# Kernel optimization log

Measured on AMD Instinct MI355X. Metric: run time of the kernel, lower is better.

## Reference

```python
import jax, jax.numpy as jnp
import numpy as np

# Static configuration (matches init_kwargs)
B, C, H, W = 8, 64, 256, 256
WS = 8            # window size
HEADS = 4
DH = 16           # dim per head, HEADS*DH == C
L = WS * WS       # tokens per window
EPS_LN = 1e-5

# --- Swin relative-position index (static, numpy) ---
_coords = np.stack(np.meshgrid(np.arange(WS), np.arange(WS), indexing='ij'))  # [2,ws,ws]
_flat = _coords.reshape(2, -1)                                                # [2,L]
_rel = (_flat[:, :, None] - _flat[:, None, :]).transpose(1, 2, 0).copy()      # [L,L,2]
_rel[..., 0] += WS - 1
_rel[..., 1] += WS - 1
_rel[..., 0] *= 2 * WS - 1
REL_IDX = _rel.sum(-1)  # [L,L] ints in [0, (2ws-1)^2)


def _biasfree_ln(x, w):
    # x: [B,C,H,W]; BiasFree_LayerNorm over channel dim (biased var, no mean subtraction in scale)
    var = jnp.var(x, axis=1, keepdims=True)
    return x * jax.lax.rsqrt(var + EPS_LN) * w[None, :, None, None]


def _win_partition(t):  # [B,H,W,C] -> [N, L, C]
    t = t.reshape(B, H // WS, WS, W // WS, WS, C).transpose(0, 1, 3, 2, 4, 5)
    return t.reshape(-1, L, C)


def _win_reverse(t):  # [N, L, C] -> [B,H,W,C]
    t = t.reshape(B, H // WS, W // WS, WS, WS, C).transpose(0, 1, 3, 2, 4, 5)
    return t.reshape(B, H, W, C)


def _l2norm(t):
    # torch F.normalize(dim=-1) semantics
    n = jnp.sqrt(jnp.sum(t * t, axis=-1, keepdims=True))
    return t / jnp.maximum(n, 1e-12)


def _forward(x, illu_fea, ln1_w, ln2_w, w_qkv, b_qkv, rpb_table, w_proj, b_proj,
             temperature, w_qkv_m, w_dw, w_out_m):
    # ---------- spatial (window) attention branch ----------
    xs = _biasfree_ln(x, ln1_w).transpose(0, 2, 3, 1)          # [B,H,W,C]
    xw = _win_partition(xs)                                     # [N,L,C]
    iw = _win_partition(illu_fea.transpose(0, 2, 3, 1))         # [N,L,C]
    iw = iw.reshape(-1, L, HEADS, DH).transpose(0, 2, 1, 3)     # [N,h,L,d]

    qkv = (xw @ w_qkv + b_qkv).reshape(-1, L, 3, HEADS, DH).transpose(2, 0, 3, 1, 4)
    q, k, v = qkv[0], qkv[1], qkv[2]                            # [N,h,L,d]
    scale = DH ** (-0.5)
    attn = jnp.einsum('nhld,nhmd->nhlm', q * scale, k)          # [N,h,L,L]
    bias = rpb_table[REL_IDX.reshape(-1)].reshape(L, L, HEADS).transpose(2, 0, 1)
    attn = jax.nn.softmax(attn + bias[None], axis=-1)
    v = v * iw                                                  # illumination modulation
    out = jnp.einsum('nhlm,nhmd->nhld', attn, v)
    out = out.transpose(0, 2, 1, 3).reshape(-1, L, C) @ w_proj + b_proj
    win_out = _win_reverse(out).transpose(0, 3, 1, 2)           # [B,C,H,W]

    # ---------- channel (MDTA) attention branch ----------
    xm = _biasfree_ln(x, ln2_w)
    qkv_m = jnp.einsum('oc,bchw->bohw', w_qkv_m, xm)            # 1x1 conv, [B,3C,H,W]
    qkv_m = jax.lax.conv_general_dilated(
        qkv_m, w_dw, (1, 1), 'SAME', feature_group_count=3 * C,
        dimension_numbers=('NCHW', 'OIHW', 'NCHW'))             # depthwise 3x3
    qm, km, vm = jnp.split(qkv_m, 3, axis=1)                    # [B,C,H,W] each

    def heads(t):
        return t.reshape(B, HEADS, DH, H * W)                   # b (n d) h w -> b n d (hw)
    qm, km, vm, im = heads(qm), heads(km), heads(vm), heads(illu_fea)
    qm = _l2norm(qm)
    km = _l2norm(km)
    attn_c = jnp.einsum('bndx,bnex->bnde', qm, km) * temperature[None]  # [B,h,d,d]
    attn_c = jax.nn.softmax(attn_c, axis=-1)
    vm = vm * im                                                # illumination modulation
    out_c = jnp.einsum('bnde,bnex->bndx', attn_c, vm).reshape(B, C, H, W)
    mdta_out = jnp.einsum('oc,bchw->bohw', w_out_m, out_c)

    return x + win_out + mdta_out


def setup_inputs() -> dict:
    key = jax.random.key(0)
    ks = jax.random.split(key, 10)
    f32 = jnp.float32
    return {
        'x': jax.random.normal(ks[0], (B, C, H, W), f32),
        'illu_fea': jax.random.uniform(ks[1], (B, C, H, W), f32),
        'ln1_w': jnp.ones((C,), f32),
        'ln2_w': jnp.ones((C,), f32),
        'w_qkv': jax.random.normal(ks[2], (C, 3 * C), f32) * 0.02,
        'b_qkv': jnp.zeros((3 * C,), f32),
        'rpb_table': jax.random.normal(ks[3], ((2 * WS - 1) ** 2, HEADS), f32) * 0.02,
        'w_proj': jax.random.normal(ks[4], (C, C), f32) * 0.02,
        'b_proj': jnp.zeros((C,), f32),
        'temperature': jnp.ones((HEADS, 1, 1), f32),
        'w_qkv_m': jax.random.normal(ks[5], (3 * C, C), f32) * 0.02,
        'w_dw': jax.random.normal(ks[6], (3 * C, 1, 3, 3), f32) * 0.1,
        'w_out_m': jax.random.normal(ks[7], (C, C), f32) * 0.02,
    }


def reference(x, illu_fea, ln1_w, ln2_w, w_qkv, b_qkv, rpb_table, w_proj, b_proj,
              temperature, w_qkv_m, w_dw, w_out_m):
    return _forward(x, illu_fea, ln1_w, ln2_w, w_qkv, b_qkv, rpb_table, w_proj,
                    b_proj, temperature, w_qkv_m, w_dw, w_out_m)
```

## Files before the change

### kernel.cpp

```cpp
#include <hip/hip_runtime.h>
#include <hip/hip_bf16.h>

#define HW 65536
#define WIDTH 256
#define SP_OFF 77856768ull

typedef __attribute__((ext_vector_type(8))) short short8v;
typedef __attribute__((ext_vector_type(4))) short short4v;
typedef __attribute__((ext_vector_type(4))) float f32x4;

__device__ inline float bf2f(unsigned short u) {
  unsigned int i = ((unsigned int)u) << 16;
  float f; __builtin_memcpy(&f, &i, 4); return f;
}
__device__ inline unsigned short f2bf(float x) {
  __hip_bfloat16 h = __float2bfloat16(x);
  unsigned short u; __builtin_memcpy(&u, &h, 2); return u;
}

#define XH_IDX(p, g) ((p)*64 + ((((g) ^ ((p)&7)))<<3))
#define QC_IDX(ch, px) ((ch)*256 + ((((px)>>3) ^ ((ch)&7))<<3) + ((px)&7))
#define QCG_IDX(ch, G) ((ch)*256 + ((((G) ^ ((ch)&7)))<<3))

__device__ __forceinline__ void spatial_body(
    unsigned char* smem, int b, int grp,
    const float* __restrict__ x, const float* __restrict__ illu,
    const float* __restrict__ ln1w, const float* __restrict__ wqkv,
    const float* __restrict__ bqkv, const float* __restrict__ rpb,
    const float* __restrict__ wproj, const float* __restrict__ bproj,
    float* __restrict__ out, unsigned short* __restrict__ sp, int use_sp)
{
  unsigned short* shbuf = (unsigned short*)smem;
  unsigned short* ks    = (unsigned short*)(smem + 18432);
  unsigned short* vs    = (unsigned short*)(smem + 27648);
  unsigned short* vsT   = (unsigned short*)(smem + 36864);
  float* rs_tok         = (float*)(smem + 36864);
  unsigned short* biasx = (unsigned short*)(smem + 46080);

  unsigned short* xw = shbuf;
  unsigned short* qs = shbuf + 4608;

  const int tid = threadIdx.x;
  const float* xb = x + (size_t)b * 64 * HW;
  const float* ib = illu + (size_t)b * 64 * HW;

  const int lane = tid & 63;
  const int w = tid >> 6;
  const int fr = lane & 15;
  const int fg = lane >> 4;
  const int hb = w * 16;

  for (int i = tid; i < 16384; i += 256) {
    int w4 = i >> 12, q = (i >> 6) & 63, k = i & 63;
    int ridx = ((q >> 3) - (k >> 3) + 7) * 15 + ((q & 7) - (k & 7) + 7);
    biasx[(w4 * 64 + q) * 68 + k] = f2bf(rpb[ridx * 4 + w4]);
  }

  short8v bfq[3][2];
  float biasr[3];
  #pragma unroll
  for (int part = 0; part < 3; ++part) {
    int o = part * 64 + hb + fr;
    biasr[part] = bqkv[o];
    #pragma unroll
    for (int kh = 0; kh < 2; ++kh)
      #pragma unroll
      for (int j = 0; j < 8; ++j) {
        int c = kh * 32 + fg * 8 + j;
        bfq[part][kh][j] = (short)f2bf(wqkv[c * 192 + o] * ln1w[c]);
      }
  }
  short8v bfp[2];
  #pragma unroll
  for (int kh = 0; kh < 2; ++kh)
    #pragma unroll
    for (int j = 0; j < 8; ++j) {
      int c = kh * 32 + fg * 8 + j;
      bfp[kh][j] = (short)f2bf(wproj[c * 64 + hb + fr]);
    }

  for (int wi = 0; wi < 4; ++wi) {
    const int win = (grp << 2) + wi;
    const int h0 = (win >> 5) << 3;
    const int w0 = (win & 31) << 3;

    for (int i = tid; i < 1024; i += 256) {
      int c = i >> 4, seg = i & 15;
      int row = seg >> 1, half = (seg & 1) * 4;
      float4 v4 = *(const float4*)&xb[(size_t)c * HW + (h0 + row) * WIDTH + w0 + half];
      int p = row * 8 + half;
      xw[(p+0)*72 + c] = f2bf(v4.x);
      xw[(p+1)*72 + c] = f2bf(v4.y);
      xw[(p+2)*72 + c] = f2bf(v4.z);
      xw[(p+3)*72 + c] = f2bf(v4.w);
    }
    __syncthreads();
    {
      int l = tid >> 2, q4 = tid & 3;
      short8v v8a = *(const short8v*)&xw[l*72 + q4*16];
      short8v v8b = *(const short8v*)&xw[l*72 + q4*16 + 8];
      float s = 0.f, s2 = 0.f;
      #pragma unroll
      for (int j = 0; j < 8; ++j) {
        float va = bf2f((unsigned short)v8a[j]), vb = bf2f((unsigned short)v8b[j]);
        s += va + vb; s2 += va * va + vb * vb;
      }
      s += __shfl_down(s, 1); s2 += __shfl_down(s2, 1);
      s += __shfl_down(s, 2); s2 += __shfl_down(s2, 2);
      if (q4 == 0) {
        float mean = s * 0.015625f;
        float var = s2 * 0.015625f - mean * mean;
        rs_tok[l] = rsqrtf(var + 1e-5f);
      }
    }
    __syncthreads();
    {
      short8v a[4][2];
      #pragma unroll
      for (int rt = 0; rt < 4; ++rt)
        #pragma unroll
        for (int kh = 0; kh < 2; ++kh)
          a[rt][kh] = *(const short8v*)&xw[(rt*16 + fr)*72 + kh*32 + fg*8];
      #pragma unroll
      for (int part = 0; part < 3; ++part) {
        float bias = biasr[part];
        #pragma unroll
        for (int rt = 0; rt < 4; ++rt) {
          f32x4 acc = {0.f, 0.f, 0.f, 0.f};
          acc = __builtin_amdgcn_mfma_f32_16x16x32_bf16(a[rt][0], bfq[part][0], acc, 0, 0, 0);
          acc = __builtin_amdgcn_mfma_f32_16x16x32_bf16(a[rt][1], bfq[part][1], acc, 0, 0, 0);
          #pragma unroll
          for (int r = 0; r < 4; ++r) {
            int t = rt*16 + fg*4 + r;
            float val = acc[r] * rs_tok[t] + bias;
            if (part == 0)      qs[t*72 + hb + fr] = f2bf(val * 0.25f);
            else if (part == 1) ks[t*72 + hb + fr] = f2bf(val);
            else                vs[t*72 + hb + fr] = f2bf(val);
          }
        }
      }
    }
    __syncthreads();
    for (int i = tid; i < 1024; i += 256) {
      int c = i >> 4, seg = i & 15;
      int row = seg >> 1, half = (seg & 1) * 4;
      float4 v4 = *(const float4*)&ib[(size_t)c * HW + (h0 + row) * WIDTH + w0 + half];
      int p = row * 8 + half;
      xw[(p+0)*72 + c] = f2bf(v4.x);
      xw[(p+1)*72 + c] = f2bf(v4.y);
      xw[(p+2)*72 + c] = f2bf(v4.z);
      xw[(p+3)*72 + c] = f2bf(v4.w);
    }
    __syncthreads();
    for (int i = tid; i < 4096; i += 256) {
      int l = i >> 6, c = i & 63;
      unsigned short vb16 = f2bf(bf2f(vs[l*72 + c]) * bf2f(xw[l*72 + c]));
      vs[l*72 + c] = vb16;
      vsT[c*72 + ((((l >> 3) ^ (c & 7)) << 3) | (l & 7))] = vb16;
    }
    __syncthreads();
    float inv_s[4];
    {
      short8v zero8 = {0,0,0,0,0,0,0,0};
      short8v kf[4], qf[4];
      #pragma unroll
      for (int t = 0; t < 4; ++t) {
        if (fg < 2) {
          kf[t] = *(const short8v*)&ks[(t*16 + fr)*72 + hb + fg*8];
          qf[t] = *(const short8v*)&qs[(t*16 + fr)*72 + hb + fg*8];
        } else { kf[t] = zero8; qf[t] = zero8; }
      }
      f32x4 st[4][4];
      #pragma unroll
      for (int kt = 0; kt < 4; ++kt)
        #pragma unroll
        for (int qt = 0; qt < 4; ++qt) {
          f32x4 z = {0.f, 0.f, 0.f, 0.f};
          st[kt][qt] = __builtin_amdgcn_mfma_f32_16x16x32_bf16(kf[kt], qf[qt], z, 0, 0, 0);
        }
      float sc[4][16];
      #pragma unroll
      for (int qt = 0; qt < 4; ++qt) {
        const unsigned short* brow = &biasx[(w * 64 + qt * 16 + fr) * 68];
        float mx = -1e30f;
        #pragma unroll
        for (int kt = 0; kt < 4; ++kt) {
          short4v b4 = *(const short4v*)&brow[kt * 16 + fg * 4];
          #pragma unroll
          for (int r = 0; r < 4; ++r) {
            float v = st[kt][qt][r] + bf2f((unsigned short)b4[r]);
            sc[qt][kt*4 + r] = v;
            mx = fmaxf(mx, v);
          }
        }
        mx = fmaxf(mx, __shfl_xor(mx, 16));
        mx = fmaxf(mx, __shfl_xor(mx, 32));
        float ss = 0.f;
        #pragma unroll
        for (int j = 0; j < 16; ++j) { float e = __expf(sc[qt][j] - mx); sc[qt][j] = e; ss += e; }
        ss += __shfl_xor(ss, 16);
        ss += __shfl_xor(ss, 32);
        inv_s[qt] = 1.f / ss;
      }
      __syncthreads();
      unsigned short* pb = shbuf + w * 2304;
      f32x4 ot[4];
      #pragma unroll
      for (int nt = 0; nt < 4; ++nt) { f32x4 z = {0.f,0.f,0.f,0.f}; ot[nt] = z; }
      #pragma unroll
      for (int P = 0; P < 2; ++P) {
        #pragma unroll
        for (int qt = 0; qt < 4; ++qt)
          #pragma unroll
          for (int k2 = 0; k2 < 2; ++k2) {
            int kt = 2*P + k2;
            unsigned int lo = (unsigned)f2bf(sc[qt][kt*4+0]) | ((unsigned)f2bf(sc[qt][kt*4+1]) << 16);
            unsigned int hi = (unsigned)f2bf(sc[qt][kt*4+2]) | ((unsigned)f2bf(sc[qt][kt*4+3]) << 16);
            uint2 pk; pk.x = lo; pk.y = hi;
            *(uint2*)&pb[(qt*16 + fr)*36 + k2*16 + fg*4] = pk;
          }
        __syncthreads();
        short8v av = *(const short8v*)&vsT[(hb + fr)*72 + (((P*4 + fg) ^ ((hb + fr) & 7)) << 3)];
        #pragma unroll
        for (int nt = 0; nt < 4; ++nt) {
          short4v p0 = *(const short4v*)&pb[(nt*16 + fr)*36 + fg*8];
          short4v p1 = *(const short4v*)&pb[(nt*16 + fr)*36 + fg*8 + 4];
          short8v bv;
          #pragma unroll
          for (int j = 0; j < 4; ++j) { bv[j] = p0[j]; bv[4+j] = p1[j]; }
          ot[nt] = __builtin_amdgcn_mfma_f32_16x16x32_bf16(av, bv, ot[nt], 0, 0, 0);
        }
        __syncthreads();
      }
      #pragma unroll
      for (int nt = 0; nt < 4; ++nt) {
        float iv = inv_s[nt];
        unsigned int lo = (unsigned)f2bf(ot[nt][0]*iv) | ((unsigned)f2bf(ot[nt][1]*iv) << 16);
        unsigned int hi = (unsigned)f2bf(ot[nt][2]*iv) | ((unsigned)f2bf(ot[nt][3]*iv) << 16);
        uint2 pk; pk.x = lo; pk.y = hi;
        *(uint2*)&ks[(nt*16 + fr)*72 + hb + fg*4] = pk;
      }
    }
    __syncthreads();
    {
      short8v a[4][2];
      #pragma unroll
      for (int rt = 0; rt < 4; ++rt)
        #pragma unroll
        for (int kh = 0; kh < 2; ++kh)
          a[rt][kh] = *(const short8v*)&ks[(rt*16 + fr)*72 + kh*32 + fg*8];
      #pragma unroll
      for (int rt = 0; rt < 4; ++rt) {
        f32x4 acc = {0.f, 0.f, 0.f, 0.f};
        acc = __builtin_amdgcn_mfma_f32_16x16x32_bf16(a[rt][0], bfp[0], acc, 0, 0, 0);
        acc = __builtin_amdgcn_mfma_f32_16x16x32_bf16(a[rt][1], bfp[1], acc, 0, 0, 0);
        #pragma unroll
        for (int r = 0; r < 4; ++r)
          vs[(rt*16 + fg*4 + r)*72 + hb + fr] = f2bf(acc[r]);
      }
    }
    __syncthreads();
    if (use_sp) {
      unsigned short* spw = sp + (size_t)(b * 1024 + win) * 4096;
      for (int i = tid; i < 1024; i += 256) {
        int row = i >> 7, rem = i & 127;
        int c = rem >> 1, half = (rem & 1) * 4;
        int p = row * 8 + half;
        size_t gofs = (size_t)c * HW + (h0 + row) * WIDTH + w0 + half;
        float4 xr4 = *(const float4*)&xb[gofs];
        float bp = bproj[c];
        unsigned int lo = (unsigned)f2bf(xr4.x + bp + bf2f(vs[(p+0)*72 + c]))
                        | ((unsigned)f2bf(xr4.y + bp + bf2f(vs[(p+1)*72 + c])) << 16);
        unsigned int hi = (unsigned)f2bf(xr4.z + bp + bf2f(vs[(p+2)*72 + c]))
                        | ((unsigned)f2bf(xr4.w + bp + bf2f(vs[(p+3)*72 + c])) << 16);
        uint2 pk; pk.x = lo; pk.y = hi;
        *(uint2*)&spw[row*512 + c*8 + half] = pk;
      }
    } else {
      for (int i = tid; i < 1024; i += 256) {
        int o = i >> 4, seg = i & 15;
        int row = seg >> 1, half = (seg & 1) * 4;
        int p = row * 8 + half;
        size_t gofs = (size_t)o * HW + (h0 + row) * WIDTH + w0 + half;
        float4 xr4 = *(const float4*)&xb[gofs];
        float bp = bproj[o];
        float4 r;
        r.x = xr4.x + bp + bf2f(vs[(p+0)*72 + o]);
        r.y = xr4.y + bp + bf2f(vs[(p+1)*72 + o]);
        r.z = xr4.z + bp + bf2f(vs[(p+2)*72 + o]);
        r.w = xr4.w + bp + bf2f(vs[(p+3)*72 + o]);
        *(float4*)&out[(size_t)b * 64 * HW + gofs] = r;
      }
    }
    __syncthreads();
  }
}

__device__ __forceinline__ void chan_body(
    unsigned char* smem, int b, int tile,
    const float* __restrict__ x, const float* __restrict__ illu,
    const float* __restrict__ ln2w, const float* __restrict__ w1,
    const float* __restrict__ wdw,
    unsigned short* __restrict__ vm, float* __restrict__ Gp,
    float* __restrict__ Nqp, float* __restrict__ Nkp)
{
  unsigned short* xh = (unsigned short*)smem;
  unsigned short* tb = (unsigned short*)(smem + 41472);
  unsigned short* qc = (unsigned short*)(smem + 64512);
  unsigned short* kc = (unsigned short*)(smem + 72704);
  float* rsp = (float*)tb;

  const int tid = threadIdx.x;
  const int blk = (b << 8) | tile;
  const int ty0 = (tile >> 4) << 4, tx0 = (tile & 15) << 4;
  const float* xb = x + (size_t)b * 64 * HW;

  for (int i = tid; i < 64 * 324; i += 256) {
    int c = i / 324, p = i - c * 324;
    int hy = p / 18, hx = p - hy * 18;
    int gy = ty0 + hy - 1, gx = tx0 + hx - 1;
    float v = 0.f;
    if (gy >= 0 && gy < 256 && gx >= 0 && gx < 256)
      v = xb[(size_t)c * HW + gy * WIDTH + gx];
    xh[XH_IDX(p, c >> 3) + (c & 7)] = f2bf(v);
  }
  __syncthreads();
  for (int p = tid; p < 324; p += 256) {
    float s = 0.f, s2 = 0.f;
    #pragma unroll
    for (int g = 0; g < 8; ++g) {
      short8v v8 = *(const short8v*)&xh[XH_IDX(p, g)];
      #pragma unroll
      for (int j = 0; j < 8; ++j) { float v = bf2f((unsigned short)v8[j]); s += v; s2 += v * v; }
    }
    float mean = s * 0.015625f;
    float var = s2 * 0.015625f - mean * mean;
    rsp[p] = rsqrtf(var + 1e-5f);
  }
  __syncthreads();
  for (int i = tid; i < 2592; i += 256) {
    int p = i >> 3;
    float rs = rsp[p];
    short8v v8 = *(const short8v*)&xh[i * 8];
    #pragma unroll
    for (int j = 0; j < 8; ++j) v8[j] = (short)f2bf(bf2f((unsigned short)v8[j]) * rs);
    *(short8v*)&xh[i * 8] = v8;
  }
  __syncthreads();

  const int lane = tid & 63;
  const int wid = tid >> 6;
  const int fcol = lane & 15;
  const int fk = lane >> 4;
  const int dpy = (tid >> 2) & 15;
  const int dg = tid & 3;

  auto gemm32 = [&](int qb, int kb) {
    short8v bq[2], bk[2];
    const float* wrq = w1 + (size_t)(qb + fcol) * 64;
    const float* wrk = w1 + (size_t)(kb + fcol) * 64;
    #pragma unroll
    for (int s = 0; s < 2; ++s) {
      int cs = fk * 8 + s * 32;
      #pragma unroll
      for (int j = 0; j < 8; ++j) {
        float lw = ln2w[cs + j];
        bq[s][j] = (short)f2bf(wrq[cs + j] * lw);
        bk[s][j] = (short)f2bf(wrk[cs + j] * lw);
      }
    }
    for (int t = wid; t < 21; t += 4) {
      int ar = t * 16 + fcol;
      short8v a0, a1;
      if (ar < 324) {
        a0 = *(const short8v*)&xh[XH_IDX(ar, fk)];
        a1 = *(const short8v*)&xh[XH_IDX(ar, fk + 4)];
      } else {
        short8v z = {0,0,0,0,0,0,0,0};
        a0 = z; a1 = z;
      }
      f32x4 aq = {0.f, 0.f, 0.f, 0.f};
      f32x4 ak = {0.f, 0.f, 0.f, 0.f};
      aq = __builtin_amdgcn_mfma_f32_16x16x32_bf16(a0, bq[0], aq, 0, 0, 0);
      aq = __builtin_amdgcn_mfma_f32_16x16x32_bf16(a1, bq[1], aq, 0, 0, 0);
      ak = __builtin_amdgcn_mfma_f32_16x16x32_bf16(a0, bk[0], ak, 0, 0, 0);
      ak = __builtin_amdgcn_mfma_f32_16x16x32_bf16(a1, bk[1], ak, 0, 0, 0);
      #pragma unroll
      for (int r = 0; r < 4; ++r) {
        int px = t * 16 + fk * 4 + r;
        if (px < 324) {
          int hy = px / 18, hx = px - hy * 18;
          tb[fcol * 360 + hy * 20 + hx]        = f2bf(aq[r]);
          tb[(16 + fcol) * 360 + hy * 20 + hx] = f2bf(ak[r]);
        }
      }
    }
  };

  float dout8[8][4];
  auto dw32 = [&](int qwb, int kwb) {
    #pragma unroll
    for (int oc8 = 0; oc8 < 8; ++oc8) {
      int oc = wid * 8 + oc8;
      int ch = (oc < 16) ? (qwb + oc) : (kwb + oc - 16);
      const float* w9 = wdw + (size_t)ch * 9;
      float wk[9];
      #pragma unroll
      for (int t = 0; t < 9; ++t) wk[t] = w9[t];
      float a0 = 0.f, a1 = 0.f, a2 = 0.f, a3 = 0.f;
      #pragma unroll
      for (int ky = 0; ky < 3; ++ky) {
        int base = oc * 360 + (dpy + ky) * 20 + dg * 4;
        short4v t4 = *(const short4v*)&tb[base];
        unsigned int t2 = *(const unsigned int*)&tb[base + 4];
        float e0 = bf2f((unsigned short)t4[0]);
        float e1 = bf2f((unsigned short)t4[1]);
        float e2 = bf2f((unsigned short)t4[2]);
        float e3 = bf2f((unsigned short)t4[3]);
        float e4 = bf2f((unsigned short)(t2 & 0xffff));
        float e5 = bf2f((unsigned short)(t2 >> 16));
        float k0 = wk[ky*3+0], k1 = wk[ky*3+1], k2 = wk[ky*3+2];
        a0 += k0*e0 + k1*e1 + k2*e2;
        a1 += k0*e1 + k1*e2 + k2*e3;
        a2 += k0*e2 + k1*e3 + k2*e4;
        a3 += k0*e3 + k1*e4 + k2*e5;
      }
      dout8[oc8][0] = a0; dout8[oc8][1] = a1;
      dout8[oc8][2] = a2; dout8[oc8][3] = a3;
    }
  };

  for (int n = 0; n < 4; ++n) {
    gemm32(16 * n, 64 + 16 * n);
    __syncthreads();
    dw32(16 * n, 64 + 16 * n);
    #pragma unroll
    for (int oc8 = 0; oc8 < 8; ++oc8) {
      int oc = wid * 8 + oc8;
      unsigned short* dst = (oc < 16) ? qc : kc;
      int row = oc & 15;
      #pragma unroll
      for (int i = 0; i < 4; ++i)
        dst[QC_IDX(row, dpy*16 + dg*4 + i)] = f2bf(dout8[oc8][i]);
    }
    __syncthreads();
    {
      int ch = tid >> 4, seg = tid & 15;
      float sq = 0.f, sk = 0.f;
      #pragma unroll
      for (int j = 0; j < 16; ++j) {
        float vq = bf2f(qc[QC_IDX(ch, seg * 16 + j)]); sq += vq * vq;
        float vk = bf2f(kc[QC_IDX(ch, seg * 16 + j)]); sk += vk * vk;
      }
      sq += __shfl_xor(sq, 1); sq += __shfl_xor(sq, 2); sq += __shfl_xor(sq, 4); sq += __shfl_xor(sq, 8);
      sk += __shfl_xor(sk, 1); sk += __shfl_xor(sk, 2); sk += __shfl_xor(sk, 4); sk += __shfl_xor(sk, 8);
      if (seg == 0) {
        Nqp[(size_t)blk * 64 + n * 16 + ch] = sq;
        Nkp[(size_t)blk * 64 + n * 16 + ch] = sk;
      }
    }
    if (wid == 0) {
      f32x4 g = {0.f, 0.f, 0.f, 0.f};
      #pragma unroll
      for (int s = 0; s < 8; ++s) {
        int G = fk + 4 * s;
        short8v aq = *(const short8v*)&qc[QCG_IDX(fcol, G)];
        short8v bk = *(const short8v*)&kc[QCG_IDX(fcol, G)];
        g = __builtin_amdgcn_mfma_f32_16x16x32_bf16(aq, bk, g, 0, 0, 0);
      }
      float* gp = Gp + ((size_t)blk * 4 + n) * 256;
      #pragma unroll
      for (int r = 0; r < 4; ++r) gp[(fk * 4 + r) * 16 + fcol] = g[r];
    }
  }
  const float* ib = illu + (size_t)b * 64 * HW;
  for (int j = 0; j < 2; ++j) {
    gemm32(128 + 32 * j, 144 + 32 * j);
    __syncthreads();
    dw32(128 + 32 * j, 144 + 32 * j);
    int gy = ty0 + dpy, gx = tx0 + dg * 4;
    size_t ppos = (size_t)gy * WIDTH + gx;
    #pragma unroll
    for (int oc8 = 0; oc8 < 8; ++oc8) {
      int vc = 32 * j + wid * 8 + oc8;
      float4 iv4 = *(const float4*)&ib[(size_t)vc * HW + ppos];
      unsigned int lo = (unsigned)f2bf(dout8[oc8][0] * iv4.x)
                      | ((unsigned)f2bf(dout8[oc8][1] * iv4.y) << 16);
      unsigned int hi = (unsigned)f2bf(dout8[oc8][2] * iv4.z)
                      | ((unsigned)f2bf(dout8[oc8][3] * iv4.w) << 16);
      uint2 pk; pk.x = lo; pk.y = hi;
      *(uint2*)&vm[((size_t)b * 64 + vc) * HW + ppos] = pk;
    }
    __syncthreads();
  }
}

__global__ __launch_bounds__(256, 2) void k_fused(
    const float* __restrict__ x, const float* __restrict__ illu,
    const float* __restrict__ ln1w, const float* __restrict__ ln2w,
    const float* __restrict__ wqkv, const float* __restrict__ bqkv,
    const float* __restrict__ rpb, const float* __restrict__ wproj,
    const float* __restrict__ bproj, const float* __restrict__ w1,
    const float* __restrict__ wdw,
    float* __restrict__ out, unsigned short* __restrict__ sp, int use_sp,
    unsigned short* __restrict__ vm, float* __restrict__ Gp,
    float* __restrict__ Nqp, float* __restrict__ Nkp)
{
  __shared__ __align__(16) unsigned char smem[80896];
  const int xcd = blockIdx.x & 7;
  const int j = blockIdx.x >> 3;
  const int idx = j >> 1;
  if (j & 1)
    chan_body(smem, xcd, idx, x, illu, ln2w, w1, wdw, vm, Gp, Nqp, Nkp);
  else
    spatial_body(smem, xcd, idx, x, illu, ln1w, wqkv, bqkv, rpb, wproj, bproj, out, sp, use_sp);
}

__global__ __launch_bounds__(256) void k_reduce1(
    const float* __restrict__ Gp, const float* __restrict__ Nqp, const float* __restrict__ Nkp,
    float* __restrict__ G2, float* __restrict__ Nq2, float* __restrict__ Nk2)
{
  const int blk = blockIdx.x;
  const int b = blk >> 5, g = blk & 31;
  const int tid = threadIdx.x;
  float ga[4] = {0.f, 0.f, 0.f, 0.f};
  for (int t = 0; t < 8; ++t) {
    const float* src = Gp + ((size_t)(b * 256 + g * 8 + t)) * 1024;
    #pragma unroll
    for (int j = 0; j < 4; ++j) ga[j] += src[tid + j * 256];
  }
  float* dst = G2 + ((size_t)(b * 32 + g)) * 1024;
  #pragma unroll
  for (int j = 0; j < 4; ++j) dst[tid + j * 256] = ga[j];
  if (tid < 128) {
    int ch = tid & 63; bool isq = tid < 64;
    const float* np = isq ? Nqp : Nkp;
    float s = 0.f;
    for (int t = 0; t < 8; ++t) s += np[((size_t)(b * 256 + g * 8 + t)) * 64 + ch];
    (isq ? Nq2 : Nk2)[(size_t)(b * 32 + g) * 64 + ch] = s;
  }
}

__global__ __launch_bounds__(256) void k_reduce2(
    const float* __restrict__ G2, const float* __restrict__ Nq2, const float* __restrict__ Nk2,
    const float* __restrict__ temp, const float* __restrict__ wout, float* __restrict__ M)
{
  __shared__ float Gs[1024];
  __shared__ float As[4][16][17];
  __shared__ float nq[64], nk[64];
  const int b = blockIdx.x;
  const int tid = threadIdx.x;
  float ga[4] = {0.f, 0.f, 0.f, 0.f};
  for (int g = 0; g < 32; ++g) {
    const float* src = G2 + ((size_t)(b * 32 + g)) * 1024;
    #pragma unroll
    for (int j = 0; j < 4; ++j) ga[j] += src[tid + j * 256];
  }
  #pragma unroll
  for (int j = 0; j < 4; ++j) Gs[tid + j * 256] = ga[j];
  if (tid < 128) {
    int ch = tid & 63; bool isq = tid < 64;
    const float* n2 = isq ? Nq2 : Nk2;
    float s = 0.f;
    for (int g = 0; g < 32; ++g) s += n2[(size_t)(b * 32 + g) * 64 + ch];
    float r = fmaxf(sqrtf(s), 1e-12f);
    (isq ? nq : nk)[ch] = r;
  }
  __syncthreads();
  if (tid < 64) {
    int n = tid >> 4, d = tid & 15;
    float tv = temp[n];
    float row[16]; float mx = -1e30f;
    #pragma unroll
    for (int e = 0; e < 16; ++e) {
      float v = Gs[n * 256 + d * 16 + e] / (nq[n * 16 + d] * nk[n * 16 + e]) * tv;
      row[e] = v; mx = fmaxf(mx, v);
    }
    float s = 0.f;
    #pragma unroll
    for (int e = 0; e < 16; ++e) { float ev = __expf(row[e] - mx); row[e] = ev; s += ev; }
    float inv = 1.f / s;
    #pragma unroll
    for (int e = 0; e < 16; ++e) As[n][d][e] = row[e] * inv;
  }
  __syncthreads();
  float* Mb = M + (size_t)b * 4096;
  for (int i = tid; i < 4096; i += 256) {
    int o = i >> 6, cp = i & 63;
    int n = cp >> 4, e = cp & 15;
    float a = 0.f;
    #pragma unroll
    for (int d = 0; d < 16; ++d) a += wout[o * 64 + n * 16 + d] * As[n][d][e];
    Mb[i] = a;
  }
}

__global__ __launch_bounds__(256, 3) void k_mdta_out(
    const unsigned short* __restrict__ vm, const float* __restrict__ M,
    const unsigned short* __restrict__ sp, int use_sp,
    float* __restrict__ out)
{
  __shared__ __align__(16) float Ml[4096];
  __shared__ __align__(16) unsigned short spl[64 * 264];
  const int blk = blockIdx.x;
  const int b = blk >> 8;
  const int y = blk & 255;
  const int tid = threadIdx.x;

  const float* Mb = M + (size_t)b * 4096;
  for (int i = tid; i < 4096; i += 256) Ml[i] = Mb[i];
  if (use_sp) {
    int wy = y >> 3, py = y & 7;
    const unsigned short* spb = sp + ((((size_t)b * 1024 + wy * 32) * 8) + py) * 512;
    for (int k = 0; k < 8; ++k) {
      int i3 = k * 256 + tid;
      int o = i3 & 63, wx = i3 >> 6;
      short8v v8 = *(const short8v*)&spb[(size_t)wx * 4096 + o * 8];
      *(short8v*)&spl[o * 264 + wx * 8] = v8;
    }
  }
  __syncthreads();
  float xcol[64];
  const unsigned short* vb = vm + (size_t)b * 64 * HW + y * 256 + tid;
  #pragma unroll
  for (int c = 0; c < 64; ++c) xcol[c] = bf2f(vb[(size_t)c * HW]);
  float* ob = out + (size_t)b * 64 * HW + y * 256 + tid;
  for (int o = 0; o < 64; ++o) {
    const float4* mr = (const float4*)&Ml[o * 64];
    float acc = 0.f;
    #pragma unroll
    for (int g = 0; g < 16; ++g) {
      float4 m4 = mr[g];
      acc += m4.x * xcol[g*4] + m4.y * xcol[g*4+1] + m4.z * xcol[g*4+2] + m4.w * xcol[g*4+3];
    }
    if (use_sp) ob[(size_t)o * HW] = bf2f(spl[o * 264 + tid]) + acc;
    else        ob[(size_t)o * HW] += acc;
  }
}

extern "C" void kernel_launch(void* const* d_in, const int* in_sizes, int n_in,
                              void* d_out, int out_size, void* d_ws, size_t ws_size,
                              hipStream_t stream) {
  const float* x     = (const float*)d_in[0];
  const float* illu  = (const float*)d_in[1];
  const float* ln1w  = (const float*)d_in[2];
  const float* ln2w  = (const float*)d_in[3];
  const float* wqkv  = (const float*)d_in[4];
  const float* bqkv  = (const float*)d_in[5];
  const float* rpb   = (const float*)d_in[6];
  const float* wproj = (const float*)d_in[7];
  const float* bproj = (const float*)d_in[8];
  const float* temp  = (const float*)d_in[9];
  const float* w1    = (const float*)d_in[10];
  const float* wdw   = (const float*)d_in[11];
  const float* wout  = (const float*)d_in[12];
  float* out = (float*)d_out;

  char* ws = (char*)d_ws;
  unsigned short* vm = (unsigned short*)ws;
  float* Gp  = (float*)(ws + 67108864);
  float* Nqp = (float*)(ws + 75497472);
  float* Nkp = (float*)(ws + 76021760);
  float* G2  = (float*)(ws + 76546048);
  float* Nq2 = (float*)(ws + 77594624);
  float* Nk2 = (float*)(ws + 77660160);
  float* M   = (float*)(ws + 77725696);
  unsigned short* sp = (unsigned short*)(ws + SP_OFF);
  int use_sp = (ws_size >= SP_OFF + 67108864ull) ? 1 : 0;

  k_fused<<<4096, 256, 0, stream>>>(x, illu, ln1w, ln2w, wqkv, bqkv, rpb, wproj, bproj,
                                    w1, wdw, out, sp, use_sp, vm, Gp, Nqp, Nkp);
  k_reduce1<<<256, 256, 0, stream>>>(Gp, Nqp, Nkp, G2, Nq2, Nk2);
  k_reduce2<<<8, 256, 0, stream>>>(G2, Nq2, Nk2, temp, wout, M);
  k_mdta_out<<<2048, 256, 0, stream>>>(vm, M, sp, use_sp, out);
}
```

Before: 645.8 us.

## Prefetch next window inputs into registers and drop redundant barriers in spatial attention

The spatial window loop now keeps x tiles in registers, reusing them for the residual add instead of reloading from global memory. It also prefetches the illumination tile and the next window's x tile ahead of the compute phases, so global load latency overlaps with the MFMA work. Two __syncthreads around the per-wave P·V staging buffer are removed because each wave only uses its own region. The cost is higher register pressure from the 12 float4 buffers, which could lower occupancy.

```diff
diff --git a/kernel.cpp b/kernel.cpp
--- a/kernel.cpp
+++ b/kernel.cpp
@@ -79,22 +79,44 @@
       bfp[kh][j] = (short)f2bf(wproj[c * 64 + hb + fr]);
     }
 
+  int row_[4], c_[4], half_[4], p_[4];
+  #pragma unroll
+  for (int k = 0; k < 4; ++k) {
+    int i = k * 256 + tid;
+    row_[k] = i >> 7;
+    int rem = i & 127;
+    c_[k] = rem >> 1;
+    half_[k] = (rem & 1) * 4;
+    p_[k] = row_[k] * 8 + half_[k];
+  }
+
+  float4 xregs[4], iregs[4], xnext[4];
+  {
+    const int win0 = grp << 2;
+    const int h0 = (win0 >> 5) << 3, w0 = (win0 & 31) << 3;
+    #pragma unroll
+    for (int k = 0; k < 4; ++k)
+      xregs[k] = *(const float4*)&xb[(size_t)c_[k]*HW + (h0+row_[k])*WIDTH + w0 + half_[k]];
+  }
+
   for (int wi = 0; wi < 4; ++wi) {
     const int win = (grp << 2) + wi;
     const int h0 = (win >> 5) << 3;
     const int w0 = (win & 31) << 3;
 
-    for (int i = tid; i < 1024; i += 256) {
-      int c = i >> 4, seg = i & 15;
-      int row = seg >> 1, half = (seg & 1) * 4;
-      float4 v4 = *(const float4*)&xb[(size_t)c * HW + (h0 + row) * WIDTH + w0 + half];
-      int p = row * 8 + half;
+    #pragma unroll
+    for (int k = 0; k < 4; ++k) {
+      float4 v4 = xregs[k];
+      int p = p_[k], c = c_[k];
       xw[(p+0)*72 + c] = f2bf(v4.x);
       xw[(p+1)*72 + c] = f2bf(v4.y);
       xw[(p+2)*72 + c] = f2bf(v4.z);
       xw[(p+3)*72 + c] = f2bf(v4.w);
     }
     __syncthreads();
+    #pragma unroll
+    for (int k = 0; k < 4; ++k)
+      iregs[k] = *(const float4*)&ib[(size_t)c_[k]*HW + (h0+row_[k])*WIDTH + w0 + half_[k]];
     {
       int l = tid >> 2, q4 = tid & 3;
       short8v v8a = *(const short8v*)&xw[l*72 + q4*16];
@@ -141,11 +163,10 @@
       }
     }
     __syncthreads();
-    for (int i = tid; i < 1024; i += 256) {
-      int c = i >> 4, seg = i & 15;
-      int row = seg >> 1, half = (seg & 1) * 4;
-      float4 v4 = *(const float4*)&ib[(size_t)c * HW + (h0 + row) * WIDTH + w0 + half];
-      int p = row * 8 + half;
+    #pragma unroll
+    for (int k = 0; k < 4; ++k) {
+      float4 v4 = iregs[k];
+      int p = p_[k], c = c_[k];
       xw[(p+0)*72 + c] = f2bf(v4.x);
       xw[(p+1)*72 + c] = f2bf(v4.y);
       xw[(p+2)*72 + c] = f2bf(v4.z);
@@ -159,6 +180,13 @@
       vsT[c*72 + ((((l >> 3) ^ (c & 7)) << 3) | (l & 7))] = vb16;
     }
     __syncthreads();
+    if (wi < 3) {
+      const int winn = win + 1;
+      const int hn = (winn >> 5) << 3, wn = (winn & 31) << 3;
+      #pragma unroll
+      for (int k = 0; k < 4; ++k)
+        xnext[k] = *(const float4*)&xb[(size_t)c_[k]*HW + (hn+row_[k])*WIDTH + wn + half_[k]];
+    }
     float inv_s[4];
     {
       short8v zero8 = {0,0,0,0,0,0,0,0};
@@ -219,7 +247,6 @@
             uint2 pk; pk.x = lo; pk.y = hi;
             *(uint2*)&pb[(qt*16 + fr)*36 + k2*16 + fg*4] = pk;
           }
-        __syncthreads();
         short8v av = *(const short8v*)&vsT[(hb + fr)*72 + (((P*4 + fg) ^ ((hb + fr) & 7)) << 3)];
         #pragma unroll
         for (int nt = 0; nt < 4; ++nt) {
@@ -230,7 +257,6 @@
           for (int j = 0; j < 4; ++j) { bv[j] = p0[j]; bv[4+j] = p1[j]; }
           ot[nt] = __builtin_amdgcn_mfma_f32_16x16x32_bf16(av, bv, ot[nt], 0, 0, 0);
         }
-        __syncthreads();
       }
       #pragma unroll
       for (int nt = 0; nt < 4; ++nt) {
@@ -262,12 +288,10 @@
     __syncthreads();
     if (use_sp) {
       unsigned short* spw = sp + (size_t)(b * 1024 + win) * 4096;
-      for (int i = tid; i < 1024; i += 256) {
-        int row = i >> 7, rem = i & 127;
-        int c = rem >> 1, half = (rem & 1) * 4;
-        int p = row * 8 + half;
-        size_t gofs = (size_t)c * HW + (h0 + row) * WIDTH + w0 + half;
-        float4 xr4 = *(const float4*)&xb[gofs];
+      #pragma unroll
+      for (int k = 0; k < 4; ++k) {
+        float4 xr4 = xregs[k];
+        int row = row_[k], c = c_[k], half = half_[k], p = p_[k];
         float bp = bproj[c];
         unsigned int lo = (unsigned)f2bf(xr4.x + bp + bf2f(vs[(p+0)*72 + c]))
                         | ((unsigned)f2bf(xr4.y + bp + bf2f(vs[(p+1)*72 + c])) << 16);
@@ -277,22 +301,23 @@
         *(uint2*)&spw[row*512 + c*8 + half] = pk;
       }
     } else {
-      for (int i = tid; i < 1024; i += 256) {
-        int o = i >> 4, seg = i & 15;
-        int row = seg >> 1, half = (seg & 1) * 4;
-        int p = row * 8 + half;
-        size_t gofs = (size_t)o * HW + (h0 + row) * WIDTH + w0 + half;
-        float4 xr4 = *(const float4*)&xb[gofs];
-        float bp = bproj[o];
+      #pragma unroll
+      for (int k = 0; k < 4; ++k) {
+        float4 xr4 = xregs[k];
+        int row = row_[k], c = c_[k], half = half_[k], p = p_[k];
+        size_t gofs = (size_t)c * HW + (h0 + row) * WIDTH + w0 + half;
+        float bp = bproj[c];
         float4 r;
-        r.x = xr4.x + bp + bf2f(vs[(p+0)*72 + o]);
-        r.y = xr4.y + bp + bf2f(vs[(p+1)*72 + o]);
-        r.z = xr4.z + bp + bf2f(vs[(p+2)*72 + o]);
-        r.w = xr4.w + bp + bf2f(vs[(p+3)*72 + o]);
+        r.x = xr4.x + bp + bf2f(vs[(p+0)*72 + c]);
+        r.y = xr4.y + bp + bf2f(vs[(p+1)*72 + c]);
+        r.z = xr4.z + bp + bf2f(vs[(p+2)*72 + c]);
+        r.w = xr4.w + bp + bf2f(vs[(p+3)*72 + c]);
         *(float4*)&out[(size_t)b * 64 * HW + gofs] = r;
       }
     }
     __syncthreads();
+    #pragma unroll
+    for (int k = 0; k < 4; ++k) xregs[k] = xnext[k];
   }
 }
 
```

New measurement: 652.8 us. Within noise of the previous version (+1.1%).
